# Optimization experiments

Measured on AMD Instinct MI355X. Metric: run time of the kernel, lower is better.

The kernel has to match this reference:

```python
import jax, jax.numpy as jnp
import numpy as np

N = 100000
E = 800000
NFEAT = 128
NHID = 128
NCLASS = 40
THRESHOLD = 0.1
EPS = 1e-8


def setup_inputs() -> dict:
    key = jax.random.key(0)
    ks = jax.random.split(key, 12)
    x = jax.random.normal(ks[0], (N, NFEAT), dtype=jnp.float32)
    edge_index = jax.random.randint(ks[1], (2, E), 0, N, dtype=jnp.int64)
    edge_index2 = jax.random.randint(ks[2], (2, E), 0, N, dtype=jnp.int64)
    s1 = 1.0 / np.sqrt(NFEAT)
    s2 = 1.0 / np.sqrt(NHID)
    s3 = 1.0 / np.sqrt(NCLASS)
    W_gc1 = jax.random.uniform(ks[3], (NFEAT, NHID), jnp.float32, -s1, s1)
    b_gc1 = jax.random.uniform(ks[4], (NHID,), jnp.float32, -s1, s1)
    W_gc2 = jax.random.uniform(ks[5], (NHID, NCLASS), jnp.float32, -s2, s2)
    b_gc2 = jax.random.uniform(ks[6], (NCLASS,), jnp.float32, -s2, s2)
    W_att1 = jax.random.uniform(ks[7], (NCLASS, NCLASS), jnp.float32, -s3, s3)
    b_att1 = jax.random.uniform(ks[8], (NCLASS,), jnp.float32, -s3, s3)
    W_att2 = jax.random.uniform(ks[9], (NCLASS, 1), jnp.float32, -s3, s3)
    return {"x": x, "W_gc1": W_gc1, "b_gc1": b_gc1, "W_gc2": W_gc2,
            "b_gc2": b_gc2, "W_att1": W_att1, "b_att1": b_att1,
            "W_att2": W_att2, "edge_index": edge_index, "edge_index2": edge_index2}


def att_coef(feat, row, col, alive):
    # cosine similarity per edge; edges failing the threshold get weight 0
    # (exactly equivalent to removing them: contribute 0 to degree & messages).
    a = feat[row]          # [E, d]
    b = feat[col]          # [E, d]
    dot = jnp.sum(a * b, axis=-1)
    na = jnp.maximum(jnp.linalg.norm(a, axis=-1), EPS)
    nb = jnp.maximum(jnp.linalg.norm(b, axis=-1), EPS)
    sims = dot / (na * nb)
    mask = alive & (sims >= THRESHOLD)
    # original computes this under torch.no_grad()
    ew = jax.lax.stop_gradient(jnp.where(mask, sims, 0.0))
    return ew, mask


def gcn_conv(x, row, col, ew, W, b):
    # PyG GCNConv with add_self_loops=True, normalize=True on weighted adjacency
    h = x @ W                                     # [N, out]
    deg = jax.ops.segment_sum(ew, row, num_segments=N) + 1.0  # +1 self loop
    dinv = deg ** -0.5
    nw = dinv[row] * ew * dinv[col]               # [E]
    agg = jax.ops.segment_sum(h[col] * nw[:, None], row, num_segments=N)
    agg = agg + h * (dinv * dinv)[:, None]        # self-loop contribution
    return agg + b


def reference(x, W_gc1, b_gc1, W_gc2, b_gc2, W_att1, b_att1, W_att2,
              edge_index, edge_index2):
    r1, c1 = edge_index[0], edge_index[1]
    r2, c2 = edge_index2[0], edge_index2[1]
    ones = jnp.ones((E,), dtype=bool)

    ew2, m2 = att_coef(x, r2, c2, ones)
    ew1, m1 = att_coef(x, r1, c1, ones)

    x2 = jax.nn.relu(gcn_conv(x, r2, c2, ew2, W_gc1, b_gc1))
    x1 = jax.nn.relu(gcn_conv(x, r1, c1, ew1, W_gc1, b_gc1))
    # dropout is identity at eval time

    ew2b, _ = att_coef(x2, r2, c2, m2)
    ew1b, _ = att_coef(x1, r1, c1, m1)

    x2 = gcn_conv(x2, r2, c2, ew2b, W_gc2, b_gc2)
    x1 = gcn_conv(x1, r1, c1, ew1b, W_gc2, b_gc2)

    z = jnp.stack([x1, x2], axis=1)               # [N, 2, C]
    w = jnp.tanh(z @ W_att1 + b_att1) @ W_att2    # [N, 2, 1]
    beta = jax.nn.softmax(w, axis=1)
    fused = jnp.sum(beta * z, axis=1)             # [N, C]
    return jax.nn.log_softmax(fused, axis=1)
```

## Files before the change

kernel.cpp:

```cpp
#include <hip/hip_runtime.h>
#include <hip/hip_bf16.h>

#define NN 100000
#define EE 800000
#define THRV 0.1f
#define DELTA 0.008f
#define EPSV 1e-8f

#define ATOMIC_ADD_F32 unsafeAtomicAdd

__device__ inline int dot4(int a, int b, int c) {
#if __has_builtin(__builtin_amdgcn_sdot4)
    return __builtin_amdgcn_sdot4(a, b, c, false);
#else
    int s = c;
    #pragma unroll
    for (int k = 0; k < 4; k++) {
        int av = (a << (24 - 8 * k)) >> 24;
        int bv = (b << (24 - 8 * k)) >> 24;
        s += av * bv;
    }
    return s;
#endif
}

__device__ inline unsigned short f2bf(float f) {
    unsigned int u = __float_as_uint(f);
    u += 0x7fffu + ((u >> 16) & 1u);
    return (unsigned short)(u >> 16);
}

__device__ inline float bf2f(unsigned short s) {
    return __uint_as_float(((unsigned int)s) << 16);
}


__global__ __launch_bounds__(256) void normalize_k(const float* __restrict__ x,
                                                   unsigned short* __restrict__ xq,
                                                   float* __restrict__ rs,
                                                   float* __restrict__ norms_x,
                                                   float* __restrict__ degL1) {
    int node = blockIdx.x * 4 + (threadIdx.x >> 6);
    int lane = threadIdx.x & 63;
    float2 v = reinterpret_cast<const float2*>(x)[(size_t)node * 64 + lane];
    float ss = v.x * v.x + v.y * v.y;
    float am = fmaxf(fabsf(v.x), fabsf(v.y));
    #pragma unroll
    for (int off = 32; off; off >>= 1) {
        ss += __shfl_xor(ss, off);
        am = fmaxf(am, __shfl_xor(am, off));
    }
    float norm = fmaxf(sqrtf(ss), EPSV);
    am = fmaxf(am, 1e-12f);
    float qs = 127.0f / am;
    int q0 = __float2int_rn(v.x * qs);
    int q1 = __float2int_rn(v.y * qs);
    unsigned short packed = (unsigned short)((q0 & 0xff) | ((q1 & 0xff) << 8));
    xq[(size_t)node * 64 + lane] = packed;
    if (lane == 0) {
        norms_x[node] = norm;
        rs[node] = am / (127.0f * norm);
        degL1[node] = 1.0f;
        degL1[node + NN] = 1.0f;
    }
}


__global__ __launch_bounds__(256) void edge_sim1_k(
        const unsigned short* __restrict__ xq, const float* __restrict__ rs,
        const float* __restrict__ x, const float* __restrict__ norms_x,
        const int* __restrict__ r1, const int* __restrict__ c1,
        const int* __restrict__ r2, const int* __restrict__ c2,
        float* __restrict__ ews, float* __restrict__ degL1,
        int* __restrict__ cnt) {
    int tid = threadIdx.x;
    int e = blockIdx.x * 32 + (tid >> 3);
    int q = tid & 7;
    int rnode, cnode, gr;
    if (e < EE) { rnode = r1[e]; cnode = c1[e]; gr = rnode; }
    else { int ee = e - EE; rnode = r2[ee]; cnode = c2[ee]; gr = NN + rnode; }
    int role = q >> 2;
    int j = q & 3;
    int node = role ? cnode : rnode;
    const uint4* base = reinterpret_cast<const uint4*>(xq) + (size_t)node * 8 + j * 2;
    uint4 v0 = base[0];
    uint4 v1 = base[1];
    uint4 p0, p1;
    p0.x = (unsigned)__shfl_xor((int)v0.x, 4);
    p0.y = (unsigned)__shfl_xor((int)v0.y, 4);
    p0.z = (unsigned)__shfl_xor((int)v0.z, 4);
    p0.w = (unsigned)__shfl_xor((int)v0.w, 4);
    p1.x = (unsigned)__shfl_xor((int)v1.x, 4);
    p1.y = (unsigned)__shfl_xor((int)v1.y, 4);
    p1.z = (unsigned)__shfl_xor((int)v1.z, 4);
    p1.w = (unsigned)__shfl_xor((int)v1.w, 4);
    int d = dot4((int)v0.x, (int)p0.x, 0);
    d = dot4((int)v0.y, (int)p0.y, d);
    d = dot4((int)v0.z, (int)p0.z, d);
    d = dot4((int)v0.w, (int)p0.w, d);
    d = dot4((int)v1.x, (int)p1.x, d);
    d = dot4((int)v1.y, (int)p1.y, d);
    d = dot4((int)v1.z, (int)p1.z, d);
    d = dot4((int)v1.w, (int)p1.w, d);
    d += __shfl_xor(d, 1);
    d += __shfl_xor(d, 2);
    float sim = (float)d * rs[rnode] * rs[cnode];
    if (fabsf(sim - THRV) <= DELTA) {
        const float4* xa = reinterpret_cast<const float4*>(x + (size_t)rnode * 128);
        const float4* xb = reinterpret_cast<const float4*>(x + (size_t)cnode * 128);
        float df = 0.f;
        #pragma unroll
        for (int t = 0; t < 4; t++) {
            float4 a = xa[q + 8 * t];
            float4 b = xb[q + 8 * t];
            df += a.x * b.x + a.y * b.y + a.z * b.z + a.w * b.w;
        }
        df += __shfl_xor(df, 1);
        df += __shfl_xor(df, 2);
        df += __shfl_xor(df, 4);
        sim = df / (norms_x[rnode] * norms_x[cnode]);
    }
    float w = (sim >= THRV) ? sim : 0.0f;
    if (q == 0) {
        ews[e] = w;
        if (w != 0.0f) {
            ATOMIC_ADD_F32(&degL1[gr], w);
            atomicAdd(&cnt[gr], 1);
        }
    }
}


__global__ __launch_bounds__(512) void scan1_k(const int* __restrict__ in,
                                               int* __restrict__ out,
                                               int* __restrict__ partials, int n) {
    __shared__ int a[1024], b[1024];
    int t = threadIdx.x;
    int base = blockIdx.x * 1024;
    a[t]       = (base + t       < n) ? in[base + t]       : 0;
    a[t + 512] = (base + t + 512 < n) ? in[base + t + 512] : 0;
    __syncthreads();
    int* src = a; int* dst = b;
    for (int off = 1; off < 1024; off <<= 1) {
        #pragma unroll
        for (int q = 0; q < 2; q++) {
            int i = t + q * 512;
            int v = src[i];
            if (i >= off) v += src[i - off];
            dst[i] = v;
        }
        __syncthreads();
        int* tmp = src; src = dst; dst = tmp;
    }
    for (int q = 0; q < 2; q++) {
        int i = t + q * 512;
        if (base + i < n) out[base + i] = i ? src[i - 1] : 0;
    }
    if (t == 0) partials[blockIdx.x] = src[1023];
}

__global__ __launch_bounds__(256) void scan2_k(int* __restrict__ partials, int m) {
    __shared__ int a[256], b[256];
    int t = threadIdx.x;
    a[t] = (t < m) ? partials[t] : 0;
    __syncthreads();
    int* src = a; int* dst = b;
    for (int off = 1; off < 256; off <<= 1) {
        int v = src[t];
        if (t >= off) v += src[t - off];
        dst[t] = v;
        __syncthreads();
        int* tmp = src; src = dst; dst = tmp;
    }
    if (t < m) partials[t] = t ? src[t - 1] : 0;
}

__global__ void scan3_k(int* __restrict__ start, int* __restrict__ next,
                        const int* __restrict__ partials,
                        const int* __restrict__ cnt, int n) {
    int i = blockIdx.x * 256 + threadIdx.x;
    if (i < n) {
        int v = start[i] + partials[i >> 10];
        start[i] = v;
        next[i] = v;
        if (i == n - 1) start[n] = v + cnt[i];
    }
}


__global__ void scatter_alive_k(const int* __restrict__ r1, const int* __restrict__ c1,
                                const int* __restrict__ r2, const int* __restrict__ c2,
                                const float* __restrict__ ews,
                                const float* __restrict__ degL1,
                                int* __restrict__ next, int2* __restrict__ acw) {
    int e = blockIdx.x * 256 + threadIdx.x;
    float w = ews[e];
    if (w == 0.0f) return;
    int gr, c, sb;
    if (e < EE) { gr = r1[e]; c = c1[e]; sb = 0; }
    else        { gr = NN + r2[e - EE]; c = c2[e - EE]; sb = NN; }
    int pos = atomicAdd(&next[gr], 1);
    int2 rec;
    rec.x = c;
    rec.y = __float_as_int(w * rsqrtf(degL1[sb + c]));
    acw[pos] = rec;
}


__global__ __launch_bounds__(256) void gemm_nh_k(const float* __restrict__ A,
                                                 const float* __restrict__ W,
                                                 unsigned short* __restrict__ Cb, int n) {
    __shared__ float Ws[64 * 128];
    __shared__ float Xs[32 * 64];
    int tid = threadIdx.x;
    int row0 = blockIdx.x * 32;
    int cg = tid & 31;
    int rl = tid >> 5;
    float4 acc[4];
    #pragma unroll
    for (int i = 0; i < 4; i++) acc[i] = make_float4(0.f, 0.f, 0.f, 0.f);

    for (int kt = 0; kt < 2; kt++) {
        const float4* Wg = reinterpret_cast<const float4*>(W + kt * 64 * 128);
        float4* Ws4 = reinterpret_cast<float4*>(Ws);
        #pragma unroll
        for (int i = 0; i < 8; i++) Ws4[tid + 256 * i] = Wg[tid + 256 * i];
        float4* Xs4 = reinterpret_cast<float4*>(Xs);
        #pragma unroll
        for (int i = 0; i < 2; i++) {
            int idx = tid + 256 * i;
            int rr = idx >> 4, kq = idx & 15;
            int grow = row0 + rr; if (grow >= n) grow = n - 1;
            Xs4[idx] = reinterpret_cast<const float4*>(A + (size_t)grow * 128 + kt * 64)[kq];
        }
        __syncthreads();
        for (int k = 0; k < 64; k++) {
            float4 wv = reinterpret_cast<const float4*>(Ws + k * 128)[cg];
            #pragma unroll
            for (int r4 = 0; r4 < 4; r4++) {
                float xv = Xs[(rl + 8 * r4) * 64 + k];
                acc[r4].x += xv * wv.x; acc[r4].y += xv * wv.y;
                acc[r4].z += xv * wv.z; acc[r4].w += xv * wv.w;
            }
        }
        __syncthreads();
    }
    #pragma unroll
    for (int r4 = 0; r4 < 4; r4++) {
        int grow = row0 + rl + 8 * r4;
        if (grow < n) {
            ushort4 o;
            o.x = f2bf(acc[r4].x); o.y = f2bf(acc[r4].y);
            o.z = f2bf(acc[r4].z); o.w = f2bf(acc[r4].w);
            reinterpret_cast<ushort4*>(Cb + (size_t)grow * 128)[cg] = o;
        }
    }
}


__global__ __launch_bounds__(256) void gemm_nc_k(const float* __restrict__ A,
                                                 const float* __restrict__ W,
                                                 float* __restrict__ C, int n) {
    __shared__ float Ws[128 * 40];
    __shared__ float Xs[64 * 130];
    int tid = threadIdx.x;
    int row0 = blockIdx.x * 64;
    for (int i = tid; i < 128 * 40; i += 256) Ws[i] = W[i];
    #pragma unroll
    for (int i = 0; i < 8; i++) {
        int idx = tid + 256 * i;
        int rr = idx >> 5, kq = idx & 31;
        int grow = row0 + rr; if (grow >= n) grow = n - 1;
        float4 v = reinterpret_cast<const float4*>(A + (size_t)grow * 128)[kq];
        float* dst = &Xs[rr * 130 + kq * 4];
        dst[0] = v.x; dst[1] = v.y; dst[2] = v.z; dst[3] = v.w;
    }
    __syncthreads();
    int c5 = tid & 7;
    int r  = tid >> 3;
    float acc0[5] = {0, 0, 0, 0, 0}, acc1[5] = {0, 0, 0, 0, 0};
    for (int k = 0; k < 128; k++) {
        float x0 = Xs[r * 130 + k], x1 = Xs[(r + 32) * 130 + k];
        #pragma unroll
        for (int c = 0; c < 5; c++) {
            float wv = Ws[k * 40 + c5 * 5 + c];
            acc0[c] += x0 * wv; acc1[c] += x1 * wv;
        }
    }
    int g0 = row0 + r, g1 = row0 + r + 32;
    if (g0 < n) {
        for (int c = 0; c < 5; c++) C[(size_t)g0 * 40 + c5 * 5 + c] = acc0[c];
    }
    if (g1 < n) {
        for (int c = 0; c < 5; c++) C[(size_t)g1 * 40 + c5 * 5 + c] = acc1[c];
    }
}


__global__ __launch_bounds__(256) void agg128_fused_k(
        const unsigned short* __restrict__ hb, const int* __restrict__ start,
        const int2* __restrict__ acw, const float* __restrict__ degL1,
        const float* __restrict__ bias, float* __restrict__ agg,
        float* __restrict__ norms_l2, float* __restrict__ degL2) {
    int gr = blockIdx.x * 4 + (threadIdx.x >> 6);
    int lane = threadIdx.x & 63;
    int rnode = (gr < NN) ? gr : gr - NN;
    int j0 = start[gr], j1 = start[gr + 1];
    float2 acc = make_float2(0.f, 0.f);
    for (int j = j0; j < j1; j++) {
        int2 rec = acw[j];
        float wv = __int_as_float(rec.y);
        unsigned int hv = reinterpret_cast<const unsigned int*>(hb)
                              [(size_t)rec.x * 64 + lane];
        acc.x += bf2f((unsigned short)(hv & 0xffff)) * wv;
        acc.y += bf2f((unsigned short)(hv >> 16)) * wv;
    }
    float dr = rsqrtf(degL1[gr]);
    unsigned int hs = reinterpret_cast<const unsigned int*>(hb)
                          [(size_t)rnode * 64 + lane];
    float hx = bf2f((unsigned short)(hs & 0xffff));
    float hy = bf2f((unsigned short)(hs >> 16));
    float2 bb = reinterpret_cast<const float2*>(bias)[lane];
    float vx = fmaxf(acc.x * dr + hx * dr * dr + bb.x, 0.0f);
    float vy = fmaxf(acc.y * dr + hy * dr * dr + bb.y, 0.0f);
    reinterpret_cast<float2*>(agg)[(size_t)gr * 64 + lane] = make_float2(vx, vy);
    float ss = vx * vx + vy * vy;
    #pragma unroll
    for (int off = 32; off; off >>= 1) ss += __shfl_xor(ss, off);
    if (lane == 0) {
        norms_l2[gr] = fmaxf(sqrtf(ss), EPSV);
        degL2[gr] = 1.0f;
    }
}


__global__ __launch_bounds__(256) void edge_sim2_k(
        const float* __restrict__ agg, const float* __restrict__ norms_l2,
        const int* __restrict__ start, int2* __restrict__ acw,
        float* __restrict__ degL2) {
    int gr = blockIdx.x * 4 + (threadIdx.x >> 6);
    int lane = threadIdx.x & 63;
    int j0 = start[gr], j1 = start[gr + 1];
    if (j0 == j1) return;
    int set_base = (gr < NN) ? 0 : NN;
    float2 a = reinterpret_cast<const float2*>(agg)[(size_t)gr * 64 + lane];
    float nr = norms_l2[gr];
    float sum = 0.f;
    for (int j = j0; j < j1; j++) {
        int2 rec = acw[j];
        int cg = set_base + rec.x;
        float2 b = reinterpret_cast<const float2*>(agg)[(size_t)cg * 64 + lane];
        float d = a.x * b.x + a.y * b.y;
        #pragma unroll
        for (int off = 32; off; off >>= 1) d += __shfl_xor(d, off);
        float sim = d / (nr * norms_l2[cg]);
        float w2 = (sim >= THRV) ? sim : 0.0f;
        if (lane == 0) acw[j].y = __float_as_int(w2);
        sum += w2;
    }
    if (lane == 0) degL2[gr] = 1.0f + sum;
}


__global__ __launch_bounds__(256) void agg40_fused_k(
        const float* __restrict__ h2, const int* __restrict__ start,
        const int2* __restrict__ acw, const float* __restrict__ degL2,
        const float* __restrict__ bias, float* __restrict__ aggy) {
    int gr = blockIdx.x * 4 + (threadIdx.x >> 6);
    int lane = threadIdx.x & 63;
    int set_base = (gr < NN) ? 0 : NN;
    int j0 = start[gr], j1 = start[gr + 1];
    bool act = lane < 40;
    float acc = 0.f;
    for (int j = j0; j < j1; j++) {
        int2 rec = acw[j];
        float w2 = __int_as_float(rec.y);
        if (w2 == 0.0f) continue;
        int cg = set_base + rec.x;
        float nv = w2 * rsqrtf(degL2[cg]);
        if (act) acc += h2[(size_t)cg * 40 + lane] * nv;
    }
    if (act) {
        float dr = rsqrtf(degL2[gr]);
        float self = h2[(size_t)gr * 40 + lane];
        aggy[(size_t)gr * 40 + lane] = acc * dr + self * dr * dr + bias[lane];
    }
}


__global__ __launch_bounds__(256) void fusion_k(const float* __restrict__ y1,
                                                const float* __restrict__ y2,
                                                const float* __restrict__ W1,
                                                const float* __restrict__ b1,
                                                const float* __restrict__ W2,
                                                float* __restrict__ out, int n) {
    __shared__ float W1s[40 * 40];
    __shared__ float b1s[40];
    __shared__ float W2s[40];
    int tid = threadIdx.x;
    for (int i = tid; i < 1600; i += 256) W1s[i] = W1[i];
    if (tid < 40) { b1s[tid] = b1[tid]; W2s[tid] = W2[tid]; }
    __syncthreads();
    int i = blockIdx.x * 256 + tid;
    if (i >= n) return;
    float z1[40], z2[40];
    const float4* y14 = reinterpret_cast<const float4*>(y1 + (size_t)i * 40);
    const float4* y24 = reinterpret_cast<const float4*>(y2 + (size_t)i * 40);
    #pragma unroll
    for (int q = 0; q < 10; q++) {
        float4 a = y14[q], b = y24[q];
        z1[4 * q] = a.x; z1[4 * q + 1] = a.y; z1[4 * q + 2] = a.z; z1[4 * q + 3] = a.w;
        z2[4 * q] = b.x; z2[4 * q + 1] = b.y; z2[4 * q + 2] = b.z; z2[4 * q + 3] = b.w;
    }
    float w1 = 0.f, w2 = 0.f;
    for (int c = 0; c < 40; c++) {
        float s1 = b1s[c], s2 = b1s[c];
        for (int j = 0; j < 40; j++) {
            float ww = W1s[j * 40 + c];
            s1 += z1[j] * ww; s2 += z2[j] * ww;
        }
        float wa = W2s[c];
        w1 += tanhf(s1) * wa; w2 += tanhf(s2) * wa;
    }
    float m = fmaxf(w1, w2);
    float e1 = expf(w1 - m), e2 = expf(w2 - m);
    float inv = 1.0f / (e1 + e2);
    float be1 = e1 * inv, be2 = e2 * inv;
    float fu[40];
    float mx = -1e30f;
    #pragma unroll
    for (int c = 0; c < 40; c++) {
        fu[c] = be1 * z1[c] + be2 * z2[c];
        mx = fmaxf(mx, fu[c]);
    }
    float se = 0.f;
    #pragma unroll
    for (int c = 0; c < 40; c++) se += expf(fu[c] - mx);
    float ls = logf(se);
    float4* o4 = reinterpret_cast<float4*>(out + (size_t)i * 40);
    #pragma unroll
    for (int q = 0; q < 10; q++) {
        float4 v;
        v.x = fu[4 * q] - mx - ls; v.y = fu[4 * q + 1] - mx - ls;
        v.z = fu[4 * q + 2] - mx - ls; v.w = fu[4 * q + 3] - mx - ls;
        o4[q] = v;
    }
}


extern "C" void kernel_launch(void* const* d_in, const int* in_sizes, int n_in,
                              void* d_out, int out_size, void* d_ws, size_t ws_size,
                              hipStream_t stream) {
    (void)in_sizes; (void)n_in; (void)out_size; (void)ws_size;
    const float* x   = (const float*)d_in[0];
    const float* Wg1 = (const float*)d_in[1];
    const float* bg1 = (const float*)d_in[2];
    const float* Wg2 = (const float*)d_in[3];
    const float* bg2 = (const float*)d_in[4];
    const float* Wa1 = (const float*)d_in[5];
    const float* ba1 = (const float*)d_in[6];
    const float* Wa2 = (const float*)d_in[7];
    const int* ei1 = (const int*)d_in[8];
    const int* ei2 = (const int*)d_in[9];
    const int *r1 = ei1, *c1 = ei1 + EE;
    const int *r2 = ei2, *c2 = ei2 + EE;
    float* out = (float*)d_out;

    float* wp = (float*)d_ws;
    float* norms_x  = wp;  wp += NN;
    float* norms_l2 = wp;  wp += 2 * NN;
    float* rs       = wp;  wp += NN;
    float* degL1    = wp;  wp += 2 * NN;
    float* degL2    = wp;  wp += 2 * NN;
    int*   cnt      = (int*)wp;  wp += 2 * NN;
    int*   start    = (int*)wp;  wp += 2 * NN + 8;
    int*   next     = (int*)wp;  wp += 2 * NN;
    int*   partials = (int*)wp;  wp += 512;
    float* ews      = wp;  wp += 2 * EE;
    int2*  acw      = (int2*)wp; wp += (size_t)2 * 2 * EE;
    unsigned short* hb = (unsigned short*)wp; wp += (size_t)NN * 64;
    float* h2       = wp;  wp += (size_t)2 * NN * 40;
    float* agg      = wp;  wp += (size_t)2 * NN * 128;
    unsigned short* xq = (unsigned short*)agg;
    float* aggy = agg;

    const int twoN = 2 * NN;
    const int twoE = 2 * EE;
    const int scan_blocks = (twoN + 1023) / 1024;

    (void)hipMemsetAsync(cnt, 0, sizeof(int) * twoN, stream);
    normalize_k<<<NN / 4, 256, 0, stream>>>(x, xq, rs, norms_x, degL1);
    edge_sim1_k<<<twoE / 32, 256, 0, stream>>>(xq, rs, x, norms_x,
                                               r1, c1, r2, c2, ews, degL1, cnt);

    scan1_k<<<scan_blocks, 512, 0, stream>>>(cnt, start, partials, twoN);
    scan2_k<<<1, 256, 0, stream>>>(partials, scan_blocks);
    scan3_k<<<(twoN + 255) / 256, 256, 0, stream>>>(start, next, partials, cnt, twoN);
    scatter_alive_k<<<twoE / 256, 256, 0, stream>>>(r1, c1, r2, c2, ews, degL1,
                                                    next, acw);

    gemm_nh_k<<<NN / 32, 256, 0, stream>>>(x, Wg1, hb, NN);
    agg128_fused_k<<<twoN / 4, 256, 0, stream>>>(hb, start, acw, degL1, bg1,
                                                 agg, norms_l2, degL2);

    edge_sim2_k<<<twoN / 4, 256, 0, stream>>>(agg, norms_l2, start, acw, degL2);
    gemm_nc_k<<<twoN / 64, 256, 0, stream>>>(agg, Wg2, h2, twoN);
    agg40_fused_k<<<twoN / 4, 256, 0, stream>>>(h2, start, acw, degL2, bg2, aggy);

    fusion_k<<<(NN + 255) / 256, 256, 0, stream>>>(aggy, aggy + (size_t)NN * 40,
                                                   Wa1, ba1, Wa2, out, NN);
}
```

Baseline: 461.7 us.

## Quantize layer-2 features to int8/bf16 and narrow edge_sim1 to four lanes per edge

The first-layer aggregation output is now stored as bf16 along with an int8-quantized copy and a per-node scale. The second-layer edge similarity uses an int8 dot product and falls back to bf16 only for edges near the threshold. The class GEMM reads bf16 input and writes bf16 output padded to a 64-element row stride. edge_sim1 now handles each edge with 4 threads instead of 8, doubling the edges per block. Together these cut gather bandwidth in the memory-bound edge and aggregation kernels, at the cost of bf16 rounding in the hidden and class features, which risks small accuracy drift.

```diff
diff --git a/kernel.cpp b/kernel.cpp
--- a/kernel.cpp
+++ b/kernel.cpp
@@ -74,50 +74,61 @@
         float* __restrict__ ews, float* __restrict__ degL1,
         int* __restrict__ cnt) {
     int tid = threadIdx.x;
-    int e = blockIdx.x * 32 + (tid >> 3);
-    int q = tid & 7;
+    int e = blockIdx.x * 64 + (tid >> 2);
+    int q = tid & 3;
     int rnode, cnode, gr;
     if (e < EE) { rnode = r1[e]; cnode = c1[e]; gr = rnode; }
     else { int ee = e - EE; rnode = r2[ee]; cnode = c2[ee]; gr = NN + rnode; }
-    int role = q >> 2;
-    int j = q & 3;
+    int role = q >> 1;
+    int j = q & 1;
     int node = role ? cnode : rnode;
-    const uint4* base = reinterpret_cast<const uint4*>(xq) + (size_t)node * 8 + j * 2;
+    const uint4* base = reinterpret_cast<const uint4*>(xq) + (size_t)node * 8 + j * 4;
     uint4 v0 = base[0];
     uint4 v1 = base[1];
-    uint4 p0, p1;
-    p0.x = (unsigned)__shfl_xor((int)v0.x, 4);
-    p0.y = (unsigned)__shfl_xor((int)v0.y, 4);
-    p0.z = (unsigned)__shfl_xor((int)v0.z, 4);
-    p0.w = (unsigned)__shfl_xor((int)v0.w, 4);
-    p1.x = (unsigned)__shfl_xor((int)v1.x, 4);
-    p1.y = (unsigned)__shfl_xor((int)v1.y, 4);
-    p1.z = (unsigned)__shfl_xor((int)v1.z, 4);
-    p1.w = (unsigned)__shfl_xor((int)v1.w, 4);
-    int d = dot4((int)v0.x, (int)p0.x, 0);
-    d = dot4((int)v0.y, (int)p0.y, d);
-    d = dot4((int)v0.z, (int)p0.z, d);
-    d = dot4((int)v0.w, (int)p0.w, d);
-    d = dot4((int)v1.x, (int)p1.x, d);
-    d = dot4((int)v1.y, (int)p1.y, d);
-    d = dot4((int)v1.z, (int)p1.z, d);
-    d = dot4((int)v1.w, (int)p1.w, d);
+    uint4 v2 = base[2];
+    uint4 v3 = base[3];
+    int d = 0;
+    {
+        uint4 p;
+        p.x = (unsigned)__shfl_xor((int)v0.x, 2);
+        p.y = (unsigned)__shfl_xor((int)v0.y, 2);
+        p.z = (unsigned)__shfl_xor((int)v0.z, 2);
+        p.w = (unsigned)__shfl_xor((int)v0.w, 2);
+        d = dot4((int)v0.x, (int)p.x, d); d = dot4((int)v0.y, (int)p.y, d);
+        d = dot4((int)v0.z, (int)p.z, d); d = dot4((int)v0.w, (int)p.w, d);
+        p.x = (unsigned)__shfl_xor((int)v1.x, 2);
+        p.y = (unsigned)__shfl_xor((int)v1.y, 2);
+        p.z = (unsigned)__shfl_xor((int)v1.z, 2);
+        p.w = (unsigned)__shfl_xor((int)v1.w, 2);
+        d = dot4((int)v1.x, (int)p.x, d); d = dot4((int)v1.y, (int)p.y, d);
+        d = dot4((int)v1.z, (int)p.z, d); d = dot4((int)v1.w, (int)p.w, d);
+        p.x = (unsigned)__shfl_xor((int)v2.x, 2);
+        p.y = (unsigned)__shfl_xor((int)v2.y, 2);
+        p.z = (unsigned)__shfl_xor((int)v2.z, 2);
+        p.w = (unsigned)__shfl_xor((int)v2.w, 2);
+        d = dot4((int)v2.x, (int)p.x, d); d = dot4((int)v2.y, (int)p.y, d);
+        d = dot4((int)v2.z, (int)p.z, d); d = dot4((int)v2.w, (int)p.w, d);
+        p.x = (unsigned)__shfl_xor((int)v3.x, 2);
+        p.y = (unsigned)__shfl_xor((int)v3.y, 2);
+        p.z = (unsigned)__shfl_xor((int)v3.z, 2);
+        p.w = (unsigned)__shfl_xor((int)v3.w, 2);
+        d = dot4((int)v3.x, (int)p.x, d); d = dot4((int)v3.y, (int)p.y, d);
+        d = dot4((int)v3.z, (int)p.z, d); d = dot4((int)v3.w, (int)p.w, d);
+    }
     d += __shfl_xor(d, 1);
-    d += __shfl_xor(d, 2);
     float sim = (float)d * rs[rnode] * rs[cnode];
     if (fabsf(sim - THRV) <= DELTA) {
         const float4* xa = reinterpret_cast<const float4*>(x + (size_t)rnode * 128);
         const float4* xb = reinterpret_cast<const float4*>(x + (size_t)cnode * 128);
         float df = 0.f;
         #pragma unroll
-        for (int t = 0; t < 4; t++) {
-            float4 a = xa[q + 8 * t];
-            float4 b = xb[q + 8 * t];
+        for (int t = 0; t < 8; t++) {
+            float4 a = xa[q + 4 * t];
+            float4 b = xb[q + 4 * t];
             df += a.x * b.x + a.y * b.y + a.z * b.z + a.w * b.w;
         }
         df += __shfl_xor(df, 1);
         df += __shfl_xor(df, 2);
-        df += __shfl_xor(df, 4);
         sim = df / (norms_x[rnode] * norms_x[cnode]);
     }
     float w = (sim >= THRV) ? sim : 0.0f;
@@ -258,49 +269,11 @@
 }
 
 
-__global__ __launch_bounds__(256) void gemm_nc_k(const float* __restrict__ A,
-                                                 const float* __restrict__ W,
-                                                 float* __restrict__ C, int n) {
-    __shared__ float Ws[128 * 40];
-    __shared__ float Xs[64 * 130];
-    int tid = threadIdx.x;
-    int row0 = blockIdx.x * 64;
-    for (int i = tid; i < 128 * 40; i += 256) Ws[i] = W[i];
-    #pragma unroll
-    for (int i = 0; i < 8; i++) {
-        int idx = tid + 256 * i;
-        int rr = idx >> 5, kq = idx & 31;
-        int grow = row0 + rr; if (grow >= n) grow = n - 1;
-        float4 v = reinterpret_cast<const float4*>(A + (size_t)grow * 128)[kq];
-        float* dst = &Xs[rr * 130 + kq * 4];
-        dst[0] = v.x; dst[1] = v.y; dst[2] = v.z; dst[3] = v.w;
-    }
-    __syncthreads();
-    int c5 = tid & 7;
-    int r  = tid >> 3;
-    float acc0[5] = {0, 0, 0, 0, 0}, acc1[5] = {0, 0, 0, 0, 0};
-    for (int k = 0; k < 128; k++) {
-        float x0 = Xs[r * 130 + k], x1 = Xs[(r + 32) * 130 + k];
-        #pragma unroll
-        for (int c = 0; c < 5; c++) {
-            float wv = Ws[k * 40 + c5 * 5 + c];
-            acc0[c] += x0 * wv; acc1[c] += x1 * wv;
-        }
-    }
-    int g0 = row0 + r, g1 = row0 + r + 32;
-    if (g0 < n) {
-        for (int c = 0; c < 5; c++) C[(size_t)g0 * 40 + c5 * 5 + c] = acc0[c];
-    }
-    if (g1 < n) {
-        for (int c = 0; c < 5; c++) C[(size_t)g1 * 40 + c5 * 5 + c] = acc1[c];
-    }
-}
-
-
 __global__ __launch_bounds__(256) void agg128_fused_k(
         const unsigned short* __restrict__ hb, const int* __restrict__ start,
         const int2* __restrict__ acw, const float* __restrict__ degL1,
-        const float* __restrict__ bias, float* __restrict__ agg,
+        const float* __restrict__ bias, unsigned int* __restrict__ aggb,
+        unsigned short* __restrict__ xq2, float* __restrict__ rs2,
         float* __restrict__ norms_l2, float* __restrict__ degL2) {
     int gr = blockIdx.x * 4 + (threadIdx.x >> 6);
     int lane = threadIdx.x & 63;
@@ -323,19 +296,32 @@
     float2 bb = reinterpret_cast<const float2*>(bias)[lane];
     float vx = fmaxf(acc.x * dr + hx * dr * dr + bb.x, 0.0f);
     float vy = fmaxf(acc.y * dr + hy * dr * dr + bb.y, 0.0f);
-    reinterpret_cast<float2*>(agg)[(size_t)gr * 64 + lane] = make_float2(vx, vy);
+    aggb[(size_t)gr * 64 + lane] =
+        (unsigned int)f2bf(vx) | ((unsigned int)f2bf(vy) << 16);
     float ss = vx * vx + vy * vy;
-    #pragma unroll
-    for (int off = 32; off; off >>= 1) ss += __shfl_xor(ss, off);
+    float am = fmaxf(vx, vy);
+    #pragma unroll
+    for (int off = 32; off; off >>= 1) {
+        ss += __shfl_xor(ss, off);
+        am = fmaxf(am, __shfl_xor(am, off));
+    }
+    float norm = fmaxf(sqrtf(ss), EPSV);
+    am = fmaxf(am, 1e-12f);
+    float qs = 127.0f / am;
+    int q0 = __float2int_rn(vx * qs);
+    int q1 = __float2int_rn(vy * qs);
+    xq2[(size_t)gr * 64 + lane] = (unsigned short)((q0 & 0xff) | ((q1 & 0xff) << 8));
     if (lane == 0) {
-        norms_l2[gr] = fmaxf(sqrtf(ss), EPSV);
+        rs2[gr] = am / (127.0f * norm);
+        norms_l2[gr] = norm;
         degL2[gr] = 1.0f;
     }
 }
 
 
 __global__ __launch_bounds__(256) void edge_sim2_k(
-        const float* __restrict__ agg, const float* __restrict__ norms_l2,
+        const unsigned short* __restrict__ xq2, const float* __restrict__ rs2,
+        const unsigned int* __restrict__ aggb, const float* __restrict__ norms_l2,
         const int* __restrict__ start, int2* __restrict__ acw,
         float* __restrict__ degL2) {
     int gr = blockIdx.x * 4 + (threadIdx.x >> 6);
@@ -343,17 +329,33 @@
     int j0 = start[gr], j1 = start[gr + 1];
     if (j0 == j1) return;
     int set_base = (gr < NN) ? 0 : NN;
-    float2 a = reinterpret_cast<const float2*>(agg)[(size_t)gr * 64 + lane];
+    unsigned int au = xq2[(size_t)gr * 64 + lane];
+    int a0 = ((int)(au << 24)) >> 24;
+    int a1 = ((int)((au << 16) & 0xff000000u)) >> 24;
+    float ra = rs2[gr];
     float nr = norms_l2[gr];
     float sum = 0.f;
     for (int j = j0; j < j1; j++) {
         int2 rec = acw[j];
         int cg = set_base + rec.x;
-        float2 b = reinterpret_cast<const float2*>(agg)[(size_t)cg * 64 + lane];
-        float d = a.x * b.x + a.y * b.y;
+        unsigned int bu = xq2[(size_t)cg * 64 + lane];
+        int b0 = ((int)(bu << 24)) >> 24;
+        int b1 = ((int)((bu << 16) & 0xff000000u)) >> 24;
+        int d = a0 * b0 + a1 * b1;
         #pragma unroll
         for (int off = 32; off; off >>= 1) d += __shfl_xor(d, off);
-        float sim = d / (nr * norms_l2[cg]);
+        float sim = (float)d * ra * rs2[cg];
+        if (fabsf(sim - THRV) <= DELTA) {
+            unsigned int av = aggb[(size_t)gr * 64 + lane];
+            unsigned int bv = aggb[(size_t)cg * 64 + lane];
+            float df = bf2f((unsigned short)(av & 0xffff)) *
+                       bf2f((unsigned short)(bv & 0xffff)) +
+                       bf2f((unsigned short)(av >> 16)) *
+                       bf2f((unsigned short)(bv >> 16));
+            #pragma unroll
+            for (int off = 32; off; off >>= 1) df += __shfl_xor(df, off);
+            sim = df / (nr * norms_l2[cg]);
+        }
         float w2 = (sim >= THRV) ? sim : 0.0f;
         if (lane == 0) acw[j].y = __float_as_int(w2);
         sum += w2;
@@ -362,8 +364,56 @@
 }
 
 
+__global__ __launch_bounds__(256) void gemm_nc_k(const unsigned short* __restrict__ Ab,
+                                                 const float* __restrict__ W,
+                                                 unsigned short* __restrict__ Cb, int n) {
+    __shared__ float Ws[128 * 40];
+    __shared__ float Xs[64 * 130];
+    int tid = threadIdx.x;
+    int row0 = blockIdx.x * 64;
+    for (int i = tid; i < 128 * 40; i += 256) Ws[i] = W[i];
+    #pragma unroll
+    for (int i = 0; i < 4; i++) {
+        int idx = tid + 256 * i;
+        int rr = idx >> 4, kq = idx & 15;
+        int grow = row0 + rr; if (grow >= n) grow = n - 1;
+        uint4 v = reinterpret_cast<const uint4*>(Ab + (size_t)grow * 128)[kq];
+        float* dst = &Xs[rr * 130 + kq * 8];
+        dst[0] = bf2f((unsigned short)(v.x & 0xffff));
+        dst[1] = bf2f((unsigned short)(v.x >> 16));
+        dst[2] = bf2f((unsigned short)(v.y & 0xffff));
+        dst[3] = bf2f((unsigned short)(v.y >> 16));
+        dst[4] = bf2f((unsigned short)(v.z & 0xffff));
+        dst[5] = bf2f((unsigned short)(v.z >> 16));
+        dst[6] = bf2f((unsigned short)(v.w & 0xffff));
+        dst[7] = bf2f((unsigned short)(v.w >> 16));
+    }
+    __syncthreads();
+    int c5 = tid & 7;
+    int r  = tid >> 3;
+    float acc0[5] = {0, 0, 0, 0, 0}, acc1[5] = {0, 0, 0, 0, 0};
+    for (int k = 0; k < 128; k++) {
+        float x0 = Xs[r * 130 + k], x1 = Xs[(r + 32) * 130 + k];
+        #pragma unroll
+        for (int c = 0; c < 5; c++) {
+            float wv = Ws[k * 40 + c5 * 5 + c];
+            acc0[c] += x0 * wv; acc1[c] += x1 * wv;
+        }
+    }
+    int g0 = row0 + r, g1 = row0 + r + 32;
+    if (g0 < n) {
+        for (int c = 0; c < 5; c++)
+            Cb[(size_t)g0 * 64 + c5 * 5 + c] = f2bf(acc0[c]);
+    }
+    if (g1 < n) {
+        for (int c = 0; c < 5; c++)
+            Cb[(size_t)g1 * 64 + c5 * 5 + c] = f2bf(acc1[c]);
+    }
+}
+
+
 __global__ __launch_bounds__(256) void agg40_fused_k(
-        const float* __restrict__ h2, const int* __restrict__ start,
+        const unsigned short* __restrict__ h2b, const int* __restrict__ start,
         const int2* __restrict__ acw, const float* __restrict__ degL2,
         const float* __restrict__ bias, float* __restrict__ aggy) {
     int gr = blockIdx.x * 4 + (threadIdx.x >> 6);
@@ -378,11 +428,12 @@
         if (w2 == 0.0f) continue;
         int cg = set_base + rec.x;
         float nv = w2 * rsqrtf(degL2[cg]);
-        if (act) acc += h2[(size_t)cg * 40 + lane] * nv;
+        float hv = act ? bf2f(h2b[(size_t)cg * 64 + lane]) : 0.f;
+        acc += hv * nv;
     }
     if (act) {
         float dr = rsqrtf(degL2[gr]);
-        float self = h2[(size_t)gr * 40 + lane];
+        float self = bf2f(h2b[(size_t)gr * 64 + lane]);
         aggy[(size_t)gr * 40 + lane] = acc * dr + self * dr * dr + bias[lane];
     }
 }
@@ -478,11 +529,13 @@
     int*   partials = (int*)wp;  wp += 512;
     float* ews      = wp;  wp += 2 * EE;
     int2*  acw      = (int2*)wp; wp += (size_t)2 * 2 * EE;
-    unsigned short* hb = (unsigned short*)wp; wp += (size_t)NN * 64;
-    float* h2       = wp;  wp += (size_t)2 * NN * 40;
-    float* agg      = wp;  wp += (size_t)2 * NN * 128;
-    unsigned short* xq = (unsigned short*)agg;
-    float* aggy = agg;
+    unsigned short* hb  = (unsigned short*)wp; wp += (size_t)NN * 64;
+    unsigned short* h2b = (unsigned short*)wp; wp += (size_t)2 * NN * 32;
+    unsigned int*   aggb = (unsigned int*)wp;  wp += (size_t)2 * NN * 64;
+    unsigned short* xq2 = (unsigned short*)wp; wp += (size_t)2 * NN * 32;
+    unsigned short* xq = (unsigned short*)aggb;
+    float* rs2  = ews;
+    float* aggy = (float*)aggb;
 
     const int twoN = 2 * NN;
     const int twoE = 2 * EE;
@@ -490,7 +543,7 @@
 
     (void)hipMemsetAsync(cnt, 0, sizeof(int) * twoN, stream);
     normalize_k<<<NN / 4, 256, 0, stream>>>(x, xq, rs, norms_x, degL1);
-    edge_sim1_k<<<twoE / 32, 256, 0, stream>>>(xq, rs, x, norms_x,
+    edge_sim1_k<<<twoE / 64, 256, 0, stream>>>(xq, rs, x, norms_x,
                                                r1, c1, r2, c2, ews, degL1, cnt);
 
     scan1_k<<<scan_blocks, 512, 0, stream>>>(cnt, start, partials, twoN);
@@ -501,11 +554,13 @@
 
     gemm_nh_k<<<NN / 32, 256, 0, stream>>>(x, Wg1, hb, NN);
     agg128_fused_k<<<twoN / 4, 256, 0, stream>>>(hb, start, acw, degL1, bg1,
-                                                 agg, norms_l2, degL2);
-
-    edge_sim2_k<<<twoN / 4, 256, 0, stream>>>(agg, norms_l2, start, acw, degL2);
-    gemm_nc_k<<<twoN / 64, 256, 0, stream>>>(agg, Wg2, h2, twoN);
-    agg40_fused_k<<<twoN / 4, 256, 0, stream>>>(h2, start, acw, degL2, bg2, aggy);
+                                                 aggb, xq2, rs2, norms_l2, degL2);
+
+    edge_sim2_k<<<twoN / 4, 256, 0, stream>>>(xq2, rs2, aggb, norms_l2,
+                                              start, acw, degL2);
+    gemm_nc_k<<<twoN / 64, 256, 0, stream>>>((const unsigned short*)aggb, Wg2,
+                                             h2b, twoN);
+    agg40_fused_k<<<twoN / 4, 256, 0, stream>>>(h2b, start, acw, degL2, bg2, aggy);
 
     fusion_k<<<(NN + 255) / 256, 256, 0, stream>>>(aggy, aggy + (size_t)NN * 40,
                                                    Wa1, ba1, Wa2, out, NN);
```

Result: no change. 466.2 us (+1.0%).
